# Kernel optimization log

Measured on AMD Instinct MI355X. Metric: run time of the kernel, lower is better.

Reference implementation:

```python
import jax, jax.numpy as jnp
import numpy as np

WS = 8      # window_size
NH = 6      # num_heads
SHIFT = 4   # shift_size


def setup_inputs() -> dict:
    key = jax.random.key(0)
    k0, k1, k2, k3, k4 = jax.random.split(key, 5)
    B, C, H, W = 4, 192, 224, 224
    x = jax.random.normal(k0, (B, C, H, W), jnp.float32)
    # 1x1 convs == per-pixel linear layers: store weights as (out, in)
    w_qkv = jax.random.normal(k1, (3 * C, C), jnp.float32) * 0.05
    b_qkv = jax.random.normal(k2, (3 * C,), jnp.float32) * 0.05
    w_proj = jax.random.normal(k3, (C, C), jnp.float32) * 0.05
    b_proj = jax.random.normal(k4, (C,), jnp.float32) * 0.05
    return {"x": x, "w_qkv": w_qkv, "b_qkv": b_qkv, "w_proj": w_proj, "b_proj": b_proj}


def reference(x, w_qkv, b_qkv, w_proj, b_proj):
    B, C, H, W = x.shape
    hd = C // NH
    scale = hd ** -0.5

    if SHIFT > 0:
        x = jnp.roll(x, shift=(-SHIFT, -SHIFT), axis=(2, 3))

    pad_r = (WS - W % WS) % WS
    pad_b = (WS - H % WS) % WS
    if pad_r > 0 or pad_b > 0:
        x = jnp.pad(x, ((0, 0), (0, 0), (0, pad_b), (0, pad_r)))
    Hp, Wp = x.shape[2], x.shape[3]
    Hn, Wn = Hp // WS, Wp // WS

    # qkv 1x1 conv: (B,C,Hp,Wp) -> (B,3C,Hp,Wp)
    qkv = jnp.einsum('bchw,oc->bohw', x, w_qkv) + b_qkv[None, :, None, None]

    # (B,3,NH,hd,Hn,WS,Wn,WS) -> (3,B,Hn,Wn,NH,WS,WS,hd)
    qkv = qkv.reshape(B, 3, NH, hd, Hn, WS, Wn, WS)
    qkv = jnp.transpose(qkv, (1, 0, 4, 6, 2, 5, 7, 3))
    q = qkv[0].reshape(-1, NH, WS * WS, hd)  # (B*Hn*Wn, NH, 64, hd)
    k = qkv[1].reshape(-1, NH, WS * WS, hd)
    v = qkv[2].reshape(-1, NH, WS * WS, hd)

    attn = jax.nn.softmax(jnp.einsum('wnqd,wnkd->wnqk', q, k) * scale, axis=-1)
    out = jnp.einsum('wnqk,wnkd->wnqd', attn, v)

    # (B,Hn,Wn,NH,WS,WS,hd) -> (B,NH,hd,Hn,WS,Wn,WS) -> (B,C,Hp,Wp)
    out = out.reshape(B, Hn, Wn, NH, WS, WS, hd)
    out = jnp.transpose(out, (0, 3, 6, 1, 4, 2, 5)).reshape(B, C, Hp, Wp)

    out = jnp.einsum('bchw,oc->bohw', out, w_proj) + b_proj[None, :, None, None]

    if pad_r > 0 or pad_b > 0:
        out = out[:, :, :H, :W]
    if SHIFT > 0:
        out = jnp.roll(out, shift=(SHIFT, SHIFT), axis=(2, 3))
    return out
```

## Files before the change

kernel.cpp:

```cpp
#include <hip/hip_runtime.h>
#include <stdint.h>

#define HHW   224
#define CCH   192
#define SHIFT 4
#define NWIN  3136
#define NTOK  200704
#define QN    38535168ull

typedef __attribute__((ext_vector_type(8))) short bf16x8;
typedef __attribute__((ext_vector_type(4))) float f32x4;

__device__ __forceinline__ ushort f2bf(float f) {
    union { float f; uint32_t i; } v; v.f = f;
    uint32_t u = v.i;
    return (ushort)((u + 0x7FFFu + ((u >> 16) & 1u)) >> 16);
}
__device__ __forceinline__ uint32_t pk2(float a, float b) {
    return (uint32_t)f2bf(a) | ((uint32_t)f2bf(b) << 16);
}

__global__ __launch_bounds__(256) void prep_w(const float* __restrict__ w,
                                              ushort* __restrict__ wo, int nrow)
{
    int idx = blockIdx.x * 256 + threadIdx.x;
    if (idx >= nrow * 24) return;
    int rg = idx / 24, p = idx % 24;
    int ch = rg / 96, mr = rg % 96;
    int m = mr >> 4, l16 = mr & 15;
    int k = p >> 2, quad = p & 3;
    const float* src = w + (size_t)rg * 192 + p * 8;
    float4 a = *(const float4*)src;
    float4 b = *(const float4*)(src + 4);
    uint4 o;
    o.x = pk2(a.x, a.y); o.y = pk2(a.z, a.w);
    o.z = pk2(b.x, b.y); o.w = pk2(b.z, b.w);
    size_t out = (size_t)((((ch * 6 + k) * 4 + quad) * 6 + m) * 16 + l16) * 8;
    *(uint4*)(wo + out) = o;
}

__global__ __launch_bounds__(256) void prep_x(const float* __restrict__ x,
                                              ushort* __restrict__ xo)
{
    __shared__ ushort lt[1792 * 8];
    const int blk = blockIdx.x;
    const int oct = blk % 24;
    const int bh  = blk / 24;
    const int hn  = bh % 28;
    const float* xb = x + ((size_t)(bh / 28) * CCH + oct * 8) * (HHW * HHW);

    for (int u = threadIdx.x; u < 448; u += 256) {
        int r = u / 56, q = u % 56;
        int hh = (hn * 8 + r + SHIFT) % HHW;
        int ww = (q * 4 + SHIFT) % HHW;
        const float* src = xb + (size_t)hh * HHW + ww;
        float4 v[8];
        #pragma unroll
        for (int c = 0; c < 8; c++)
            v[c] = *(const float4*)(src + (size_t)c * (HHW * HHW));
        #pragma unroll
        for (int i = 0; i < 4; i++) {
            int p = u * 4 + i;
            int sw = p ^ ((p >> 3) & 7);
            uint4 o;
            o.x = pk2(((const float*)&v[0])[i], ((const float*)&v[1])[i]);
            o.y = pk2(((const float*)&v[2])[i], ((const float*)&v[3])[i]);
            o.z = pk2(((const float*)&v[4])[i], ((const float*)&v[5])[i]);
            o.w = pk2(((const float*)&v[6])[i], ((const float*)&v[7])[i]);
            *(uint4*)&lt[sw * 8] = o;
        }
    }
    __syncthreads();

    for (int u = threadIdx.x; u < 1792; u += 256) {
        int wn = u >> 6, t = u & 63;
        int p = (t >> 3) * 224 + wn * 8 + (t & 7);
        int sw = p ^ ((p >> 3) & 7);
        *(uint4*)(xo + (size_t)(bh * 28 + wn) * 12288 + oct * 512 + t * 8) =
            *(const uint4*)&lt[sw * 8];
    }
}

__global__ __launch_bounds__(384, 1) void qkv_attn_win(
    const ushort* __restrict__ xin,
    const ushort* __restrict__ wbf,
    const float* __restrict__ bias,
    ushort* __restrict__ x2o)
{
    __shared__ char smem[162816];
    char* qb = smem + 73728;
    char* kb = smem + 104448;
    char* vb = smem + 135168;

    const int tid = threadIdx.x;
    const int wave = tid / 64, lane = tid & 63;
    const int quad = lane >> 4, l16 = lane & 15;
    const int win = blockIdx.x;

    bf16x8 bfr[4][6];
    const ushort* xw = xin + (size_t)win * 12288;
    #pragma unroll
    for (int nt = 0; nt < 4; nt++)
        #pragma unroll
        for (int k = 0; k < 6; k++)
            bfr[nt][k] = *(const bf16x8*)(xw + (k * 4 + quad) * 512 + (nt * 16 + l16) * 8);

    #pragma unroll
    for (int it = 0; it < 6; it++) {
        int off = it * 3072 + wave * 512;
        __builtin_amdgcn_global_load_lds(
            (const __attribute__((address_space(1))) void*)(wbf + off + lane * 8),
            (__attribute__((address_space(3))) void*)(smem + off * 2), 16, 0, 0);
    }
    __syncthreads();

    #pragma unroll
    for (int ch = 0; ch < 6; ch++) {
        if (ch < 5) {
            const ushort* wsrc = wbf + (size_t)(ch + 1) * 18432;
            char* dbuf = smem + ((ch + 1) & 1) * 36864;
            #pragma unroll
            for (int it = 0; it < 6; it++) {
                int off = it * 3072 + wave * 512;
                __builtin_amdgcn_global_load_lds(
                    (const __attribute__((address_space(1))) void*)(wsrc + off + lane * 8),
                    (__attribute__((address_space(3))) void*)(dbuf + off * 2), 16, 0, 0);
            }
        }
        const ushort* cur = (const ushort*)(smem + (ch & 1) * 36864);

        f32x4 acc[4];
        #pragma unroll
        for (int nt = 0; nt < 4; nt++) acc[nt] = (f32x4){0.f, 0.f, 0.f, 0.f};
        #pragma unroll
        for (int k = 0; k < 6; k++) {
            bf16x8 af = *(const bf16x8*)(cur + ((k * 4 + quad) * 96 + wave * 16 + l16) * 8);
            #pragma unroll
            for (int nt = 0; nt < 4; nt++)
                acc[nt] = __builtin_amdgcn_mfma_f32_16x16x32_bf16(af, bfr[nt][k], acc[nt], 0, 0, 0);
        }

        const int o0c = ch * 96 + wave * 16 + quad * 4;
        float4 bb = *(const float4*)(bias + o0c);
        const int rem = (ch & 1) * 96 + wave * 16 + quad * 4;
        const int h = rem >> 5, d0 = rem & 31;
        #pragma unroll
        for (int nt = 0; nt < 4; nt++) {
            const int t = nt * 16 + l16;
            float f0 = acc[nt][0] + bb.x, f1 = acc[nt][1] + bb.y;
            float f2 = acc[nt][2] + bb.z, f3 = acc[nt][3] + bb.w;
            if (ch < 4) {
                char* base = (ch < 2 ? qb : kb);
                uint2 w;
                w.x = pk2(f0, f1); w.y = pk2(f2, f3);
                *(uint2*)(base + h * 5120 + t * 80 + d0 * 2) = w;
            } else {
                ushort* vh = (ushort*)(vb + h * 4608);
                vh[(d0 + 0) * 72 + t] = f2bf(f0);
                vh[(d0 + 1) * 72 + t] = f2bf(f1);
                vh[(d0 + 2) * 72 + t] = f2bf(f2);
                vh[(d0 + 3) * 72 + t] = f2bf(f3);
            }
        }
        __syncthreads();
    }

    const int h = wave;
    bf16x8 kf[4], qf[4], vf[2][2];
    #pragma unroll
    for (int nt = 0; nt < 4; nt++)
        qf[nt] = *(const bf16x8*)(qb + h * 5120 + (nt * 16 + l16) * 80 + quad * 16);
    #pragma unroll
    for (int nt = 0; nt < 4; nt++)
        kf[nt] = *(const bf16x8*)(kb + h * 5120 + (nt * 16 + l16) * 80 + quad * 16);
    #pragma unroll
    for (int md = 0; md < 2; md++)
        #pragma unroll
        for (int ks = 0; ks < 2; ks++)
            vf[md][ks] = *(const bf16x8*)(vb + h * 4608 + (md * 16 + l16) * 144 + ks * 64 + quad * 16);

    const float SC = 0.25506953149031837f;
    ushort* ph = (ushort*)smem + h * 4096;

    #pragma unroll
    for (int nq = 0; nq < 4; nq += 2) {
        f32x4 sc[2][4];
        #pragma unroll
        for (int j = 0; j < 2; j++)
            #pragma unroll
            for (int mk = 0; mk < 4; mk++) {
                sc[j][mk] = (f32x4){0.f, 0.f, 0.f, 0.f};
                sc[j][mk] = __builtin_amdgcn_mfma_f32_16x16x32_bf16(kf[mk], qf[nq + j], sc[j][mk], 0, 0, 0);
            }
        #pragma unroll
        for (int j = 0; j < 2; j++) {
            float mx = sc[j][0][0];
            #pragma unroll
            for (int mk = 0; mk < 4; mk++)
                #pragma unroll
                for (int rg = 0; rg < 4; rg++) mx = fmaxf(mx, sc[j][mk][rg]);
            mx = fmaxf(mx, __shfl_xor(mx, 16, 64));
            mx = fmaxf(mx, __shfl_xor(mx, 32, 64));
            float e[4][4];
            float sm = 0.f;
            #pragma unroll
            for (int mk = 0; mk < 4; mk++)
                #pragma unroll
                for (int rg = 0; rg < 4; rg++) {
                    e[mk][rg] = exp2f((sc[j][mk][rg] - mx) * SC);
                    sm += e[mk][rg];
                }
            sm += __shfl_xor(sm, 16, 64);
            sm += __shfl_xor(sm, 32, 64);
            float r = __builtin_amdgcn_rcpf(sm);
            const int q = (nq + j) * 16 + l16;
            const int sx = q & 7;
            ushort* row = ph + q * 64;
            #pragma unroll
            for (int mk = 0; mk < 4; mk++) {
                uint2 w;
                w.x = pk2(e[mk][0] * r, e[mk][1] * r);
                w.y = pk2(e[mk][2] * r, e[mk][3] * r);
                int s0 = mk * 2 + (quad >> 1);
                *(uint2*)(row + (((s0 ^ sx) << 3) + (quad & 1) * 4)) = w;
            }
        }
    }

    f32x4 o[2][4];
    #pragma unroll
    for (int md = 0; md < 2; md++)
        #pragma unroll
        for (int nq = 0; nq < 4; nq++) o[md][nq] = (f32x4){0.f, 0.f, 0.f, 0.f};
    #pragma unroll
    for (int ks = 0; ks < 2; ks++)
        #pragma unroll
        for (int nq = 0; nq < 4; nq++) {
            const int q = nq * 16 + l16;
            bf16x8 pf = *(const bf16x8*)(ph + q * 64 + ((((ks * 4 + quad) ^ (q & 7))) << 3));
            #pragma unroll
            for (int md = 0; md < 2; md++)
                o[md][nq] = __builtin_amdgcn_mfma_f32_16x16x32_bf16(vf[md][ks], pf, o[md][nq], 0, 0, 0);
        }

    ushort* x2 = x2o + (size_t)win * 12288;
    #pragma unroll
    for (int md = 0; md < 2; md++)
        #pragma unroll
        for (int nq = 0; nq < 4; nq++) {
            const int q = nq * 16 + l16;
            const int c = h * 32 + md * 16 + quad * 4;
            uint2 w;
            w.x = pk2(o[md][nq][0], o[md][nq][1]);
            w.y = pk2(o[md][nq][2], o[md][nq][3]);
            *(uint2*)(x2 + q * CCH + c) = w;
        }
}

__global__ __launch_bounds__(256, 3) void gemm_proj(
    const ushort* __restrict__ xin, const ushort* __restrict__ wbf,
    const float* __restrict__ bias, float* __restrict__ dout)
{
    __shared__ ushort wc[96 * 192];

    const int tid = threadIdx.x;
    const int wave = tid >> 6, lane = tid & 63;
    const int quad = lane >> 4, l16 = lane & 15;
    const int p0 = blockIdx.x * 128 + wave * 32;

    #pragma unroll
    for (int it = 0; it < 9; it++) {
        int off = (it * 4 + wave) * 512;
        __builtin_amdgcn_global_load_lds(
            (const __attribute__((address_space(1))) void*)(wbf + off + lane * 8),
            (__attribute__((address_space(3))) void*)(&wc[off]), 16, 0, 0);
    }

    bf16x8 bfr[2][6];
    #pragma unroll
    for (int nt = 0; nt < 2; nt++) {
        int token = p0 + nt * 16 + l16;
        #pragma unroll
        for (int k = 0; k < 6; k++)
            bfr[nt][k] = *(const bf16x8*)(xin + (size_t)token * CCH + k * 32 + quad * 8);
    }

    __syncthreads();

    #pragma unroll
    for (int ch = 0; ch < 2; ch++) {
        f32x4 acc[6][2];
        #pragma unroll
        for (int m = 0; m < 6; m++)
            #pragma unroll
            for (int nt = 0; nt < 2; nt++) acc[m][nt] = (f32x4){0.f, 0.f, 0.f, 0.f};

        #pragma unroll
        for (int k = 0; k < 6; k++) {
            #pragma unroll
            for (int m = 0; m < 6; m++) {
                bf16x8 afrag = *(const bf16x8*)(wc + ((k * 4 + quad) * 96 + m * 16 + l16) * 8);
                acc[m][0] = __builtin_amdgcn_mfma_f32_16x16x32_bf16(afrag, bfr[0][k], acc[m][0], 0, 0, 0);
                acc[m][1] = __builtin_amdgcn_mfma_f32_16x16x32_bf16(afrag, bfr[1][k], acc[m][1], 0, 0, 0);
            }
        }

        if (ch + 1 < 2) {
            __syncthreads();
            const ushort* wsrc = wbf + (size_t)18432;
            #pragma unroll
            for (int it = 0; it < 9; it++) {
                int off = (it * 4 + wave) * 512;
                __builtin_amdgcn_global_load_lds(
                    (const __attribute__((address_space(1))) void*)(wsrc + off + lane * 8),
                    (__attribute__((address_space(3))) void*)(&wc[off]), 16, 0, 0);
            }
        }

        const int obase = ch * 96;
        #pragma unroll
        for (int m = 0; m < 6; m++) {
            const int o0 = obase + m * 16 + quad * 4;
            float4 bb = *(const float4*)(bias + o0);
            #pragma unroll
            for (int nt = 0; nt < 2; nt++) {
                int token = p0 + nt * 16 + l16;
                int win = token >> 6, t = token & 63;
                float f0 = acc[m][nt][0] + bb.x, f1 = acc[m][nt][1] + bb.y;
                float f2 = acc[m][nt][2] + bb.z, f3 = acc[m][nt][3] + bb.w;
                int b = win / 784, hn = (win / 28) % 28, wn = win % 28;
                int hh = (hn * 8 + (t >> 3) + SHIFT) % HHW;
                int ww = (wn * 8 + (t & 7) + SHIFT) % HHW;
                float* dst = dout + ((size_t)(b * CCH + o0) * HHW + hh) * HHW + ww;
                dst[0] = f0; dst[(size_t)HHW * HHW] = f1;
                dst[2 * (size_t)HHW * HHW] = f2; dst[3 * (size_t)HHW * HHW] = f3;
            }
        }
        if (ch + 1 < 2) __syncthreads();
    }
}

extern "C" void kernel_launch(void* const* d_in, const int* in_sizes, int n_in,
                              void* d_out, int out_size, void* d_ws, size_t ws_size,
                              hipStream_t stream) {
    const float* x      = (const float*)d_in[0];
    const float* w_qkv  = (const float*)d_in[1];
    const float* b_qkv  = (const float*)d_in[2];
    const float* w_proj = (const float*)d_in[3];
    const float* b_proj = (const float*)d_in[4];
    float* out = (float*)d_out;
    ushort* ws = (ushort*)d_ws;

    ushort* X1 = (ushort*)d_out;
    ushort* WQ = (ushort*)d_out + QN;
    ushort* X2 = ws;
    ushort* WP = ws + QN;

    prep_w      <<<54, 256, 0, stream>>>(w_qkv, WQ, 576);
    prep_x      <<<4 * 28 * 24, 256, 0, stream>>>(x, X1);
    qkv_attn_win<<<NWIN, 384, 0, stream>>>(X1, WQ, b_qkv, X2);
    prep_w      <<<18, 256, 0, stream>>>(w_proj, WP, 192);
    gemm_proj   <<<NTOK / 128, 256, 0, stream>>>(X2, WP, b_proj, out);
}
```

Baseline: 506.9 us.

## Shrink attention kernel LDS for occupancy and restructure proj GEMM by image row

After: 568.3 us. +12.1%, slower.

```diff
diff --git a/kernel.cpp b/kernel.cpp
--- a/kernel.cpp
+++ b/kernel.cpp
@@ -19,15 +19,38 @@
 __device__ __forceinline__ uint32_t pk2(float a, float b) {
     return (uint32_t)f2bf(a) | ((uint32_t)f2bf(b) << 16);
 }
-
-__global__ __launch_bounds__(256) void prep_w(const float* __restrict__ w,
-                                              ushort* __restrict__ wo, int nrow)
+#define GLOAD16(src, dst) __builtin_amdgcn_global_load_lds( \
+    (const __attribute__((address_space(1))) void*)(src),   \
+    (__attribute__((address_space(3))) void*)(dst), 16, 0, 0)
+
+__global__ __launch_bounds__(256) void prep_w_qkv(const float* __restrict__ w,
+                                                  ushort* __restrict__ wo)
 {
     int idx = blockIdx.x * 256 + threadIdx.x;
-    if (idx >= nrow * 24) return;
+    if (idx >= 576 * 24) return;
     int rg = idx / 24, p = idx % 24;
-    int ch = rg / 96, mr = rg % 96;
-    int m = mr >> 4, l16 = mr & 15;
+    int s3 = rg / 192, r = rg % 192;
+    int chunk, m;
+    if (s3 == 0) { chunk = (r & 31) >> 4; m = r >> 5; }
+    else         { chunk = 2 * s3 + (r >= 96); m = (r % 96) >> 4; }
+    int li = r & 15;
+    int k = p >> 2, quad = p & 3;
+    int slice = chunk * 6 + k;
+    const float* src = w + (size_t)rg * 192 + p * 8;
+    float4 a = *(const float4*)src;
+    float4 b = *(const float4*)(src + 4);
+    uint4 o;
+    o.x = pk2(a.x, a.y); o.y = pk2(a.z, a.w);
+    o.z = pk2(b.x, b.y); o.w = pk2(b.z, b.w);
+    *(uint4*)(wo + ((size_t)slice * 384 + (quad * 6 + m) * 16 + li) * 8) = o;
+}
+
+__global__ __launch_bounds__(256) void prep_w_proj(const float* __restrict__ w,
+                                                   ushort* __restrict__ wo)
+{
+    int idx = blockIdx.x * 256 + threadIdx.x;
+    if (idx >= 192 * 24) return;
+    int rg = idx / 24, p = idx % 24;
     int k = p >> 2, quad = p & 3;
     const float* src = w + (size_t)rg * 192 + p * 8;
     float4 a = *(const float4*)src;
@@ -35,8 +58,7 @@
     uint4 o;
     o.x = pk2(a.x, a.y); o.y = pk2(a.z, a.w);
     o.z = pk2(b.x, b.y); o.w = pk2(b.z, b.w);
-    size_t out = (size_t)((((ch * 6 + k) * 4 + quad) * 6 + m) * 16 + l16) * 8;
-    *(uint4*)(wo + out) = o;
+    *(uint4*)(wo + ((((size_t)(k * 4 + quad) * 12 + (rg >> 4)) * 16 + (rg & 15))) * 8) = o;
 }
 
 __global__ __launch_bounds__(256) void prep_x(const float* __restrict__ x,
@@ -81,117 +103,139 @@
     }
 }
 
-__global__ __launch_bounds__(384, 1) void qkv_attn_win(
+__global__ __launch_bounds__(384, 3) void qkv_attn_win(
     const ushort* __restrict__ xin,
     const ushort* __restrict__ wbf,
     const float* __restrict__ bias,
     ushort* __restrict__ x2o)
 {
-    __shared__ char smem[162816];
-    char* qb = smem + 73728;
-    char* kb = smem + 104448;
-    char* vb = smem + 135168;
+    __shared__ __align__(16) char smem[79872];
+    ushort* const kl = (ushort*)(smem + 24576);
+    ushort* const vl = (ushort*)(smem + 52224);
 
     const int tid = threadIdx.x;
     const int wave = tid / 64, lane = tid & 63;
     const int quad = lane >> 4, l16 = lane & 15;
     const int win = blockIdx.x;
-
-    bf16x8 bfr[4][6];
     const ushort* xw = xin + (size_t)win * 12288;
-    #pragma unroll
-    for (int nt = 0; nt < 4; nt++)
-        #pragma unroll
-        for (int k = 0; k < 6; k++)
-            bfr[nt][k] = *(const bf16x8*)(xw + (k * 4 + quad) * 512 + (nt * 16 + l16) * 8);
-
-    #pragma unroll
-    for (int it = 0; it < 6; it++) {
-        int off = it * 3072 + wave * 512;
-        __builtin_amdgcn_global_load_lds(
-            (const __attribute__((address_space(1))) void*)(wbf + off + lane * 8),
-            (__attribute__((address_space(3))) void*)(smem + off * 2), 16, 0, 0);
+
+    {
+        const ushort* src = wbf + wave * 512 + lane * 8;
+        GLOAD16(src, smem + wave * 1024);
+        GLOAD16(src + 3072, smem + 6144 + wave * 1024);
     }
     __syncthreads();
 
+    uint32_t pq0[4][2], pq1[4][2];
+
     #pragma unroll
     for (int ch = 0; ch < 6; ch++) {
-        if (ch < 5) {
-            const ushort* wsrc = wbf + (size_t)(ch + 1) * 18432;
-            char* dbuf = smem + ((ch + 1) & 1) * 36864;
-            #pragma unroll
-            for (int it = 0; it < 6; it++) {
-                int off = it * 3072 + wave * 512;
-                __builtin_amdgcn_global_load_lds(
-                    (const __attribute__((address_space(1))) void*)(wsrc + off + lane * 8),
-                    (__attribute__((address_space(3))) void*)(dbuf + off * 2), 16, 0, 0);
-            }
-        }
-        const ushort* cur = (const ushort*)(smem + (ch & 1) * 36864);
-
-        f32x4 acc[4];
-        #pragma unroll
-        for (int nt = 0; nt < 4; nt++) acc[nt] = (f32x4){0.f, 0.f, 0.f, 0.f};
-        #pragma unroll
-        for (int k = 0; k < 6; k++) {
-            bf16x8 af = *(const bf16x8*)(cur + ((k * 4 + quad) * 96 + wave * 16 + l16) * 8);
-            #pragma unroll
-            for (int nt = 0; nt < 4; nt++)
-                acc[nt] = __builtin_amdgcn_mfma_f32_16x16x32_bf16(af, bfr[nt][k], acc[nt], 0, 0, 0);
-        }
-
-        const int o0c = ch * 96 + wave * 16 + quad * 4;
-        float4 bb = *(const float4*)(bias + o0c);
-        const int rem = (ch & 1) * 96 + wave * 16 + quad * 4;
-        const int h = rem >> 5, d0 = rem & 31;
-        #pragma unroll
-        for (int nt = 0; nt < 4; nt++) {
-            const int t = nt * 16 + l16;
-            float f0 = acc[nt][0] + bb.x, f1 = acc[nt][1] + bb.y;
-            float f2 = acc[nt][2] + bb.z, f3 = acc[nt][3] + bb.w;
-            if (ch < 4) {
-                char* base = (ch < 2 ? qb : kb);
-                uint2 w;
-                w.x = pk2(f0, f1); w.y = pk2(f2, f3);
-                *(uint2*)(base + h * 5120 + t * 80 + d0 * 2) = w;
-            } else {
-                ushort* vh = (ushort*)(vb + h * 4608);
-                vh[(d0 + 0) * 72 + t] = f2bf(f0);
-                vh[(d0 + 1) * 72 + t] = f2bf(f1);
-                vh[(d0 + 2) * 72 + t] = f2bf(f2);
-                vh[(d0 + 3) * 72 + t] = f2bf(f3);
-            }
-        }
-        __syncthreads();
+        f32x4 a[4];
+        #pragma unroll
+        for (int nt = 0; nt < 4; nt++) a[nt] = (f32x4){0.f, 0.f, 0.f, 0.f};
+        #pragma unroll
+        for (int ph3 = 0; ph3 < 3; ph3++) {
+            const int p = ch * 3 + ph3;
+            if (p < 17) {
+                const ushort* src = wbf + (size_t)(p + 1) * 6144 + wave * 512 + lane * 8;
+                char* db = smem + ((p + 1) & 1) * 12288 + wave * 1024;
+                GLOAD16(src, db);
+                GLOAD16(src + 3072, db + 6144);
+            }
+            const ushort* cb = (const ushort*)(smem + (p & 1) * 12288);
+            #pragma unroll
+            for (int sl = 0; sl < 2; sl++) {
+                const int k = ph3 * 2 + sl;
+                bf16x8 bq[4];
+                #pragma unroll
+                for (int nt = 0; nt < 4; nt++)
+                    bq[nt] = *(const bf16x8*)(xw + (k * 4 + quad) * 512 + (nt * 16 + l16) * 8);
+                bf16x8 af = *(const bf16x8*)(cb + sl * 3072 + ((quad * 6 + wave) * 16 + l16) * 8);
+                #pragma unroll
+                for (int nt = 0; nt < 4; nt++)
+                    a[nt] = __builtin_amdgcn_mfma_f32_16x16x32_bf16(af, bq[nt], a[nt], 0, 0, 0);
+            }
+            if (ph3 == 2) {
+                if (ch < 2) {
+                    float4 bb = *(const float4*)(bias + wave * 32 + ch * 16 + quad * 4);
+                    #pragma unroll
+                    for (int nt = 0; nt < 4; nt++) {
+                        uint32_t lo = pk2(a[nt][0] + bb.x, a[nt][1] + bb.y);
+                        uint32_t hi = pk2(a[nt][2] + bb.z, a[nt][3] + bb.w);
+                        if (ch == 0) { pq0[nt][0] = lo; pq0[nt][1] = hi; }
+                        else         { pq1[nt][0] = lo; pq1[nt][1] = hi; }
+                    }
+                } else if (ch < 4) {
+                    float4 bb = *(const float4*)(bias + 192 + (ch - 2) * 96 + wave * 16 + quad * 4);
+                    const int hk = (ch - 2) * 3 + (wave >> 1);
+                    const int d0 = (wave & 1) * 16 + quad * 4;
+                    #pragma unroll
+                    for (int nt = 0; nt < 4; nt++) {
+                        const int t = nt * 16 + l16;
+                        uint2 w;
+                        w.x = pk2(a[nt][0] + bb.x, a[nt][1] + bb.y);
+                        w.y = pk2(a[nt][2] + bb.z, a[nt][3] + bb.w);
+                        *(uint2*)(kl + hk * 2304 + t * 36 + d0) = w;
+                    }
+                } else {
+                    float4 bb = *(const float4*)(bias + 384 + (ch - 4) * 96 + wave * 16 + quad * 4);
+                    const int hv = (ch - 4) * 3 + (wave >> 1);
+                    const int d0 = (wave & 1) * 16 + quad * 4;
+                    ushort* vh = vl + hv * 2304;
+                    #pragma unroll
+                    for (int nt = 0; nt < 4; nt++) {
+                        const int t = nt * 16 + l16;
+                        vh[(d0 + 0) * 72 + t] = f2bf(a[nt][0] + bb.x);
+                        vh[(d0 + 1) * 72 + t] = f2bf(a[nt][1] + bb.y);
+                        vh[(d0 + 2) * 72 + t] = f2bf(a[nt][2] + bb.z);
+                        vh[(d0 + 3) * 72 + t] = f2bf(a[nt][3] + bb.w);
+                    }
+                }
+            }
+            __syncthreads();
+        }
     }
 
     const int h = wave;
-    bf16x8 kf[4], qf[4], vf[2][2];
-    #pragma unroll
-    for (int nt = 0; nt < 4; nt++)
-        qf[nt] = *(const bf16x8*)(qb + h * 5120 + (nt * 16 + l16) * 80 + quad * 16);
-    #pragma unroll
-    for (int nt = 0; nt < 4; nt++)
-        kf[nt] = *(const bf16x8*)(kb + h * 5120 + (nt * 16 + l16) * 80 + quad * 16);
+    bf16x8 kf[4], vf[2][2];
+    #pragma unroll
+    for (int mk = 0; mk < 4; mk++)
+        kf[mk] = *(const bf16x8*)(kl + h * 2304 + (mk * 16 + l16) * 36 + quad * 8);
     #pragma unroll
     for (int md = 0; md < 2; md++)
         #pragma unroll
         for (int ks = 0; ks < 2; ks++)
-            vf[md][ks] = *(const bf16x8*)(vb + h * 4608 + (md * 16 + l16) * 144 + ks * 64 + quad * 16);
+            vf[md][ks] = *(const bf16x8*)(vl + h * 2304 + (md * 16 + l16) * 72 + ks * 32 + quad * 8);
+    __syncthreads();
 
     const float SC = 0.25506953149031837f;
     ushort* ph = (ushort*)smem + h * 4096;
+    const int sl0 = ((quad & 1) << 5) + l16;
+    const int sl1 = sl0 + 16;
+    const bool hiq = quad >= 2;
 
     #pragma unroll
     for (int nq = 0; nq < 4; nq += 2) {
         f32x4 sc[2][4];
         #pragma unroll
-        for (int j = 0; j < 2; j++)
+        for (int j = 0; j < 2; j++) {
+            const int nt = nq + j;
+            uint32_t pa0 = pq0[nt][0], pa1 = pq1[nt][0];
+            uint32_t pb0 = pq0[nt][1], pb1 = pq1[nt][1];
+            uint32_t t0a = __shfl((int)pa0, sl0), t0b = __shfl((int)pa1, sl0);
+            uint32_t t1a = __shfl((int)pb0, sl0), t1b = __shfl((int)pb1, sl0);
+            uint32_t t2a = __shfl((int)pa0, sl1), t2b = __shfl((int)pa1, sl1);
+            uint32_t t3a = __shfl((int)pb0, sl1), t3b = __shfl((int)pb1, sl1);
+            uint4 u;
+            u.x = hiq ? t0b : t0a; u.y = hiq ? t1b : t1a;
+            u.z = hiq ? t2b : t2a; u.w = hiq ? t3b : t3a;
+            bf16x8 qf = *(const bf16x8*)&u;
             #pragma unroll
             for (int mk = 0; mk < 4; mk++) {
                 sc[j][mk] = (f32x4){0.f, 0.f, 0.f, 0.f};
-                sc[j][mk] = __builtin_amdgcn_mfma_f32_16x16x32_bf16(kf[mk], qf[nq + j], sc[j][mk], 0, 0, 0);
-            }
+                sc[j][mk] = __builtin_amdgcn_mfma_f32_16x16x32_bf16(kf[mk], qf, sc[j][mk], 0, 0, 0);
+            }
+        }
         #pragma unroll
         for (int j = 0; j < 2; j++) {
             float mx = sc[j][0][0];
@@ -257,86 +301,57 @@
         }
 }
 
-__global__ __launch_bounds__(256, 3) void gemm_proj(
-    const ushort* __restrict__ xin, const ushort* __restrict__ wbf,
+__global__ __launch_bounds__(384, 3) void gemm_proj(
+    const ushort* __restrict__ x2, const ushort* __restrict__ wbf,
     const float* __restrict__ bias, float* __restrict__ dout)
 {
-    __shared__ ushort wc[96 * 192];
+    __shared__ __align__(16) ushort wl[36864];
 
     const int tid = threadIdx.x;
-    const int wave = tid >> 6, lane = tid & 63;
+    const int wave = tid / 64, lane = tid & 63;
     const int quad = lane >> 4, l16 = lane & 15;
-    const int p0 = blockIdx.x * 128 + wave * 32;
-
-    #pragma unroll
-    for (int it = 0; it < 9; it++) {
-        int off = (it * 4 + wave) * 512;
-        __builtin_amdgcn_global_load_lds(
-            (const __attribute__((address_space(1))) void*)(wbf + off + lane * 8),
-            (__attribute__((address_space(3))) void*)(&wc[off]), 16, 0, 0);
-    }
-
-    bf16x8 bfr[2][6];
-    #pragma unroll
-    for (int nt = 0; nt < 2; nt++) {
-        int token = p0 + nt * 16 + l16;
-        #pragma unroll
-        for (int k = 0; k < 6; k++)
-            bfr[nt][k] = *(const bf16x8*)(xin + (size_t)token * CCH + k * 32 + quad * 8);
-    }
-
+    const int r  = blockIdx.x & 7;
+    const int bh = blockIdx.x >> 3;
+    const int b = bh / 28, hn = bh % 28;
+
+    #pragma unroll
+    for (int it = 0; it < 12; it++) {
+        const ushort* src = wbf + it * 3072 + wave * 512 + lane * 8;
+        GLOAD16(src, (char*)wl + it * 6144 + wave * 1024);
+    }
     __syncthreads();
 
-    #pragma unroll
-    for (int ch = 0; ch < 2; ch++) {
-        f32x4 acc[6][2];
-        #pragma unroll
-        for (int m = 0; m < 6; m++)
-            #pragma unroll
-            for (int nt = 0; nt < 2; nt++) acc[m][nt] = (f32x4){0.f, 0.f, 0.f, 0.f};
-
+    const int hh = (hn * 8 + r + SHIFT) % HHW;
+
+    #pragma unroll
+    for (int nt = 0; nt < 14; nt++) {
+        const int px = nt * 16 + l16;
+        const int wc = px >> 3, t7 = px & 7;
+        const ushort* bp = x2 + ((size_t)(bh * 28 + wc) * 64 + r * 8 + t7) * 192;
+        bf16x8 bq[6];
+        #pragma unroll
+        for (int k = 0; k < 6; k++) bq[k] = *(const bf16x8*)(bp + k * 32 + quad * 8);
+        f32x4 acs[2];
+        acs[0] = (f32x4){0.f, 0.f, 0.f, 0.f};
+        acs[1] = (f32x4){0.f, 0.f, 0.f, 0.f};
         #pragma unroll
         for (int k = 0; k < 6; k++) {
-            #pragma unroll
-            for (int m = 0; m < 6; m++) {
-                bf16x8 afrag = *(const bf16x8*)(wc + ((k * 4 + quad) * 96 + m * 16 + l16) * 8);
-                acc[m][0] = __builtin_amdgcn_mfma_f32_16x16x32_bf16(afrag, bfr[0][k], acc[m][0], 0, 0, 0);
-                acc[m][1] = __builtin_amdgcn_mfma_f32_16x16x32_bf16(afrag, bfr[1][k], acc[m][1], 0, 0, 0);
-            }
-        }
-
-        if (ch + 1 < 2) {
-            __syncthreads();
-            const ushort* wsrc = wbf + (size_t)18432;
-            #pragma unroll
-            for (int it = 0; it < 9; it++) {
-                int off = (it * 4 + wave) * 512;
-                __builtin_amdgcn_global_load_lds(
-                    (const __attribute__((address_space(1))) void*)(wsrc + off + lane * 8),
-                    (__attribute__((address_space(3))) void*)(&wc[off]), 16, 0, 0);
-            }
-        }
-
-        const int obase = ch * 96;
-        #pragma unroll
-        for (int m = 0; m < 6; m++) {
-            const int o0 = obase + m * 16 + quad * 4;
+            bf16x8 af0 = *(const bf16x8*)(wl + (((k * 4 + quad) * 12 + wave * 2 + 0) * 16 + l16) * 8);
+            bf16x8 af1 = *(const bf16x8*)(wl + (((k * 4 + quad) * 12 + wave * 2 + 1) * 16 + l16) * 8);
+            acs[0] = __builtin_amdgcn_mfma_f32_16x16x32_bf16(af0, bq[k], acs[0], 0, 0, 0);
+            acs[1] = __builtin_amdgcn_mfma_f32_16x16x32_bf16(af1, bq[k], acs[1], 0, 0, 0);
+        }
+        const int ww = (px + SHIFT) % HHW;
+        #pragma unroll
+        for (int mm = 0; mm < 2; mm++) {
+            const int o0 = wave * 32 + mm * 16 + quad * 4;
             float4 bb = *(const float4*)(bias + o0);
-            #pragma unroll
-            for (int nt = 0; nt < 2; nt++) {
-                int token = p0 + nt * 16 + l16;
-                int win = token >> 6, t = token & 63;
-                float f0 = acc[m][nt][0] + bb.x, f1 = acc[m][nt][1] + bb.y;
-                float f2 = acc[m][nt][2] + bb.z, f3 = acc[m][nt][3] + bb.w;
-                int b = win / 784, hn = (win / 28) % 28, wn = win % 28;
-                int hh = (hn * 8 + (t >> 3) + SHIFT) % HHW;
-                int ww = (wn * 8 + (t & 7) + SHIFT) % HHW;
-                float* dst = dout + ((size_t)(b * CCH + o0) * HHW + hh) * HHW + ww;
-                dst[0] = f0; dst[(size_t)HHW * HHW] = f1;
-                dst[2 * (size_t)HHW * HHW] = f2; dst[3 * (size_t)HHW * HHW] = f3;
-            }
-        }
-        if (ch + 1 < 2) __syncthreads();
+            float* dst = dout + (((size_t)(b * CCH + o0)) * HHW + hh) * HHW + ww;
+            dst[0]                        = acs[mm][0] + bb.x;
+            dst[(size_t)HHW * HHW]        = acs[mm][1] + bb.y;
+            dst[2 * (size_t)HHW * HHW]    = acs[mm][2] + bb.z;
+            dst[3 * (size_t)HHW * HHW]    = acs[mm][3] + bb.w;
+        }
     }
 }
 
@@ -356,9 +371,9 @@
     ushort* X2 = ws;
     ushort* WP = ws + QN;
 
-    prep_w      <<<54, 256, 0, stream>>>(w_qkv, WQ, 576);
+    prep_w_qkv  <<<54, 256, 0, stream>>>(w_qkv, WQ);
     prep_x      <<<4 * 28 * 24, 256, 0, stream>>>(x, X1);
     qkv_attn_win<<<NWIN, 384, 0, stream>>>(X1, WQ, b_qkv, X2);
-    prep_w      <<<18, 256, 0, stream>>>(w_proj, WP, 192);
-    gemm_proj   <<<NTOK / 128, 256, 0, stream>>>(X2, WP, b_proj, out);
-}
+    prep_w_proj <<<18, 256, 0, stream>>>(w_proj, WP);
+    gemm_proj   <<<4 * 28 * 8, 384, 0, stream>>>(X2, WP, b_proj, out);
+}
```
